# Kernel optimization log

Hardware: AMD Instinct MI355X
Metric: run time of the kernel (lower is better)

Reference implementation:

```python
import jax, jax.numpy as jnp
import numpy as np

I, H, C = 1024, 1024, 1000
B, S = 128, 256


def setup_inputs() -> dict:
    key = jax.random.key(0)
    ks = jax.random.split(key, 7)
    s = 1.0 / np.sqrt(H)
    u = lambda k, shape: jax.random.uniform(k, shape, jnp.float32, -s, s)
    return {
        "x": jax.random.normal(ks[0], (B, S, I), jnp.float32),
        "Wxh": u(ks[1], (4 * H, I)),   # nn.Linear(input, 4H).weight
        "bxh": u(ks[2], (4 * H,)),
        "Whh": u(ks[3], (4 * H, H)),   # nn.Linear(hidden, 4H).weight
        "bhh": u(ks[4], (4 * H,)),
        "Wfc": jax.random.normal(ks[5], (C, H), jnp.float32) / np.sqrt(H),
        "bfc": jnp.zeros((C,), jnp.float32),
    }


def reference(x, Wxh, bxh, Whh, bhh, Wfc, bfc):
    # x: [B, S, I]. Precompute input projection for all timesteps (one big GEMM).
    xW = jnp.einsum("bsi,gi->sbg", x, Wxh) + bxh + bhh  # [S, B, 4H]

    def step(carry, xw_t):
        h, c = carry
        gates = xw_t + h @ Whh.T               # [B, 4H]
        gi, gf, gg, go = jnp.split(gates, 4, axis=1)  # chunk order: i, f, chat, o
        it = jax.nn.sigmoid(gi)
        ft = jax.nn.sigmoid(gf)
        ot = jax.nn.sigmoid(go)
        chat = jnp.tanh(gg)
        c_new = c * ft + it * chat
        h_new = ot * jnp.tanh(c_new)
        return (h_new, c_new), None

    h0 = jnp.zeros((x.shape[0], H), x.dtype)
    c0 = jnp.zeros((x.shape[0], H), x.dtype)
    (h_last, _), _ = jax.lax.scan(step, (h0, c0), xW)
    return h_last @ Wfc.T + bfc  # [B, C]
```

## Files before the change

kernel.cpp:

```cpp
#include <hip/hip_runtime.h>
#include <hip/hip_bf16.h>

typedef __attribute__((ext_vector_type(8))) short short8;
typedef __attribute__((ext_vector_type(4))) float f32x4;
typedef unsigned long long u64;
typedef unsigned int u32;

#define SQLEN 256
#define BATCH 128
#define HID   1024
#define G4    4096
#define NCLS  1000

static __device__ __forceinline__ float sigm(float x){ return 1.0f/(1.0f+__expf(-x)); }
static __device__ __forceinline__ float tanhx(float x){ return 2.0f/(1.0f+__expf(-2.0f*x)) - 1.0f; }
static __device__ __forceinline__ short bf16b(float x){
  __hip_bfloat16 h = __float2bfloat16(x);
  return __builtin_bit_cast(short, h);
}
static __device__ __forceinline__ float bf2f(short s){
  return __bfloat162float(__builtin_bit_cast(__hip_bfloat16, s));
}

__global__ void cast_x_kernel(const float* __restrict__ x, short* __restrict__ xbf){
  int r = blockIdx.x;
  int s = r >> 7, b = r & 127;
  const float* src = x + ((size_t)b*SQLEN + s)*HID;
  short* dst = xbf + (size_t)r*HID;
  int k = threadIdx.x*4;
  float4 v = *(const float4*)(src + k);
  short4 o; o.x=bf16b(v.x); o.y=bf16b(v.y); o.z=bf16b(v.z); o.w=bf16b(v.w);
  *(short4*)(dst + k) = o;
}

__global__ void cast_w_kernel(const float* __restrict__ src, short* __restrict__ dst){
  int i = (blockIdx.x*256 + threadIdx.x)*4;
  float4 v = *(const float4*)(src + i);
  short4 o; o.x=bf16b(v.x); o.y=bf16b(v.y); o.z=bf16b(v.z); o.w=bf16b(v.w);
  *(short4*)(dst + i) = o;
}

__global__ void bias_kernel(const float* __restrict__ a, const float* __restrict__ b,
                            float* __restrict__ o){
  int i = blockIdx.x*256 + threadIdx.x;
  o[i] = a[i] + b[i];
}

__global__ __launch_bounds__(256,3) void gemm_xw_kernel(
    const short* __restrict__ A, const short* __restrict__ B,
    const float* __restrict__ bias, short* __restrict__ C)
{
  __shared__ __align__(16) short As[4096];
  __shared__ __align__(16) short Bs[4096];
  const int tid = threadIdx.x;
  const int swz = (((int)blockIdx.x & 7) << 10) + ((int)blockIdx.x >> 3);
  const int bm = swz >> 5;
  const int bn = swz & 31;
  const size_t r0 = (size_t)bm*128, n0 = (size_t)bn*128;
  const int lane = tid & 63, wave = tid >> 6;
  const int wm = (wave>>1)*64, wn = (wave&1)*64;
  const int l15 = lane & 15, quad = lane >> 4;

  f32x4 acc[4][4];
  #pragma unroll
  for (int m=0;m<4;++m)
    #pragma unroll
    for (int n=0;n<4;++n) acc[m][n] = (f32x4)0.0f;

  const int c0 = wave*64 + lane;
  const int c1 = c0 + 256;

  for (int kk = 0; kk < 32; ++kk){
    const int k0 = kk*32;
    __syncthreads();
    __builtin_amdgcn_global_load_lds(
        (const void*)(A + (r0 + (c0>>2))*HID + k0 + (c0&3)*8),
        (void*)((char*)As + wave*1024), 16, 0, 0);
    __builtin_amdgcn_global_load_lds(
        (const void*)(A + (r0 + (c1>>2))*HID + k0 + (c1&3)*8),
        (void*)((char*)As + 4096 + wave*1024), 16, 0, 0);
    __builtin_amdgcn_global_load_lds(
        (const void*)(B + (n0 + (c0>>2))*HID + k0 + (c0&3)*8),
        (void*)((char*)Bs + wave*1024), 16, 0, 0);
    __builtin_amdgcn_global_load_lds(
        (const void*)(B + (n0 + (c1>>2))*HID + k0 + (c1&3)*8),
        (void*)((char*)Bs + 4096 + wave*1024), 16, 0, 0);
    __syncthreads();
    short8 af[4], bf[4];
    #pragma unroll
    for (int m=0;m<4;++m) af[m] = *(const short8*)(As + (wm + m*16 + l15)*32 + quad*8);
    #pragma unroll
    for (int n=0;n<4;++n) bf[n] = *(const short8*)(Bs + (wn + n*16 + l15)*32 + quad*8);
    #pragma unroll
    for (int m=0;m<4;++m)
      #pragma unroll
      for (int n=0;n<4;++n)
        acc[m][n] = __builtin_amdgcn_mfma_f32_16x16x32_bf16(af[m], bf[n], acc[m][n], 0,0,0);
  }
  #pragma unroll
  for (int n=0;n<4;++n){
    int s = (int)n0 + wn + n*16;
    float bs = bias[s + l15];
    int g = s >> 10, jgi = (s & 1023) >> 4;
    #pragma unroll
    for (int m=0;m<4;++m){
      #pragma unroll
      for (int rg=0; rg<4; ++rg){
        u32 w0 = (u32)(unsigned short)bf16b(acc[m][n][rg] + bs);
        u32 w1 = __shfl_down(w0, 1);
        u32 w2 = __shfl_down(w0, 2);
        u32 w3 = __shfl_down(w0, 3);
        if ((l15 & 3) == 0){
          u64 pk = (u64)w0 | ((u64)w1<<16) | ((u64)w2<<32) | ((u64)w3<<48);
          int rowin = wm + m*16 + quad*4 + rg;
          *(u64*)(C + (((size_t)bm*64 + jgi)*128 + rowin)*64 + g*16 + l15) = pk;
        }
      }
    }
  }
}

__global__ __launch_bounds__(256,2) void lstm_kernel(
    const short* __restrict__ whh, const short* __restrict__ xw,
    short* __restrict__ h_all, u32* __restrict__ flags)
{
  __shared__ f32x4 part[2][4][4][64];

  const int tid  = threadIdx.x;
  const int lane = tid & 63;
  const int wave = tid >> 6;
  const int l15  = lane & 15;
  const int quad = lane >> 4;
  const int bg = blockIdx.x & 7;
  const int jg = blockIdx.x >> 3;
  const int b0 = bg*16;
  const int j0 = jg*16;
  const int ks0 = wave*256;

  __builtin_amdgcn_fence(__ATOMIC_ACQUIRE, "agent");

  short8 Bf[4][8];
  #pragma unroll
  for (int g=0; g<4; ++g)
    #pragma unroll
    for (int kit=0; kit<8; ++kit)
      Bf[g][kit] = *(const short8*)(whh + (size_t)(g*1024 + j0 + l15)*HID
                                    + ks0 + kit*32 + quad*8);

  u32* fgrp = flags + bg*64;

  const int r  = tid >> 4;
  const int jj = tid & 15;
  const int ln = (r>>2)*16 + jj;
  const int rg = r & 3;
  float cc = 0.0f;

  short xwc[4];
  {
    const short* xb = xw + (((size_t)0*64 + jg)*128 + b0 + r)*64 + jj;
    #pragma unroll
    for (int g=0; g<4; ++g) xwc[g] = xb[g*16];
  }

  for (int t = 0; t < SQLEN; ++t){
    const short* hin  = h_all + (size_t)t*131072;
    short*       hout = h_all + (size_t)(t+1)*131072;

    short xwn[4];
    if (t < SQLEN-1){
      const short* xb = xw + (((size_t)(t+1)*64 + jg)*128 + b0 + r)*64 + jj;
      #pragma unroll
      for (int g=0; g<4; ++g) xwn[g] = xb[g*16];
    }

    if (t){
      u32* fp = fgrp + wave*16 + l15;
      while (__hip_atomic_load(fp, __ATOMIC_RELAXED,
                               __HIP_MEMORY_SCOPE_AGENT) < (u32)t)
        __builtin_amdgcn_s_sleep(1);
      asm volatile("" ::: "memory");
    }

    short8 Af[8];
    #pragma unroll
    for (int kit=0; kit<8; ++kit)
      Af[kit] = *(const short8*)(hin + (size_t)(b0 + l15)*HID
                                 + ks0 + kit*32 + quad*8);

    f32x4 acc[4];
    #pragma unroll
    for (int g=0; g<4; ++g) acc[g] = (f32x4)0.0f;
    #pragma unroll
    for (int kit=0; kit<8; ++kit)
      #pragma unroll
      for (int g=0; g<4; ++g)
        acc[g] = __builtin_amdgcn_mfma_f32_16x16x32_bf16(Af[kit], Bf[g][kit], acc[g],0,0,0);

    const int pb = t & 1;
    #pragma unroll
    for (int g=0; g<4; ++g) part[pb][wave][g][lane] = acc[g];
    __syncthreads();

    float gv[4];
    #pragma unroll
    for (int g=0; g<4; ++g){
      float s = bf2f(xwc[g]);
      #pragma unroll
      for (int w=0; w<4; ++w)
        s += ((const float*)&part[pb][w][g][ln])[rg];
      gv[g] = s;
    }

    float it = sigm(gv[0]), ft = sigm(gv[1]), ch = tanhx(gv[2]), ot = sigm(gv[3]);
    cc = cc*ft + it*ch;
    float hv = ot * tanhx(cc);

    u32 w0 = (u32)(unsigned short)bf16b(hv);
    u32 w1 = __shfl_down(w0, 1);
    u32 w2 = __shfl_down(w0, 2);
    u32 w3 = __shfl_down(w0, 3);
    if (!(tid & 3)){
      u64 hp = (u64)w0 | ((u64)w1<<16) | ((u64)w2<<32) | ((u64)w3<<48);
      __hip_atomic_store((u64*)(hout + (size_t)(b0 + r)*HID + j0 + jj), hp,
                         __ATOMIC_RELAXED, __HIP_MEMORY_SCOPE_AGENT);
    }
    xwc[0]=xwn[0]; xwc[1]=xwn[1]; xwc[2]=xwn[2]; xwc[3]=xwn[3];
    __syncthreads();

    if (t < SQLEN-1 && tid == 0)
      __hip_atomic_store(fgrp + jg, (u32)(t+1), __ATOMIC_RELAXED,
                         __HIP_MEMORY_SCOPE_AGENT);
  }
}

__global__ __launch_bounds__(256) void fc_kernel(const short* __restrict__ h,
    const float* __restrict__ wfc, const float* __restrict__ bfc, float* __restrict__ out)
{
  __shared__ float hs[4][1024];
  int tid = threadIdx.x;
  int b0 = (blockIdx.x >> 3)*4;
  int cs = (blockIdx.x & 7)*125;
  for (int i = tid; i < 4096; i += 256){
    int bb = i >> 10, k = i & 1023;
    hs[bb][k] = bf2f(h[(size_t)(b0+bb)*HID + k]);
  }
  __syncthreads();
  for (int c = cs + tid; c < cs + 125; c += 256){
    const float* w = wfc + (size_t)c*HID;
    float a0=0.f,a1=0.f,a2=0.f,a3=0.f;
    for (int k=0; k<1024; k+=4){
      float4 wv = *(const float4*)(w + k);
      a0 += wv.x*hs[0][k] + wv.y*hs[0][k+1] + wv.z*hs[0][k+2] + wv.w*hs[0][k+3];
      a1 += wv.x*hs[1][k] + wv.y*hs[1][k+1] + wv.z*hs[1][k+2] + wv.w*hs[1][k+3];
      a2 += wv.x*hs[2][k] + wv.y*hs[2][k+1] + wv.z*hs[2][k+2] + wv.w*hs[2][k+3];
      a3 += wv.x*hs[3][k] + wv.y*hs[3][k+1] + wv.z*hs[3][k+2] + wv.w*hs[3][k+3];
    }
    float bb = bfc[c];
    out[(size_t)(b0+0)*NCLS + c] = a0 + bb;
    out[(size_t)(b0+1)*NCLS + c] = a1 + bb;
    out[(size_t)(b0+2)*NCLS + c] = a2 + bb;
    out[(size_t)(b0+3)*NCLS + c] = a3 + bb;
  }
}

extern "C" void kernel_launch(void* const* d_in, const int* in_sizes, int n_in,
                              void* d_out, int out_size, void* d_ws, size_t ws_size,
                              hipStream_t stream) {
  const float* x   = (const float*)d_in[0];
  const float* Wxh = (const float*)d_in[1];
  const float* bxh = (const float*)d_in[2];
  const float* Whh = (const float*)d_in[3];
  const float* bhh = (const float*)d_in[4];
  const float* Wfc = (const float*)d_in[5];
  const float* bfc = (const float*)d_in[6];
  float* out = (float*)d_out;

  char* ws = (char*)d_ws;
  short*    h_all = (short*)(ws + 0);
  short*    xbf   = (short*)(ws + 0);
  short*    wxhb  = (short*)(ws + 68157440);
  short*    whhb  = (short*)(ws + 76546048);
  float*    biasg = (float*)(ws + 84934656);
  short*    xw    = (short*)(ws + 85983232);
  u32*      flags = (u32*)(ws + 354418688);

  hipMemsetAsync(flags, 0, 4096, stream);

  cast_x_kernel<<<32768, 256, 0, stream>>>(x, xbf);
  cast_w_kernel<<<4096, 256, 0, stream>>>(Wxh, wxhb);
  cast_w_kernel<<<4096, 256, 0, stream>>>(Whh, whhb);
  bias_kernel  <<<16,   256, 0, stream>>>(bxh, bhh, biasg);
  gemm_xw_kernel<<<8192, 256, 0, stream>>>(xbf, wxhb, biasg, xw);
  hipMemsetAsync(ws, 0, 262144, stream);
  lstm_kernel  <<<512,  256, 0, stream>>>(whhb, xw, h_all, flags);
  fc_kernel    <<<256,  256, 0, stream>>>(h_all + (size_t)SQLEN*131072, Wfc, bfc, out);
}
```

Baseline: 1.599 ms.

## Enlarge xW GEMM tiles to 256x256 with double-buffered LDS prefetch

Rewrites the input-projection GEMM to use 512-thread blocks computing 256x256 output tiles with a K-step of 64. Global-to-LDS loads are double-buffered, so the next two K tiles are staged while the current one is computed, synchronised with explicit waitcnt and barrier instructions. Fragments are stored in MFMA-ready order so LDS reads are contiguous per lane. The aim is more data reuse per load and overlap of memory with MFMA work, at the cost of 128 KB of LDS and more accumulator registers per thread, which limits occupancy.

```diff
diff --git a/kernel.cpp b/kernel.cpp
--- a/kernel.cpp
+++ b/kernel.cpp
@@ -46,64 +46,91 @@
   o[i] = a[i] + b[i];
 }
 
-__global__ __launch_bounds__(256,3) void gemm_xw_kernel(
+__global__ __launch_bounds__(512,2) void gemm_xw_kernel(
     const short* __restrict__ A, const short* __restrict__ B,
     const float* __restrict__ bias, short* __restrict__ C)
 {
-  __shared__ __align__(16) short As[4096];
-  __shared__ __align__(16) short Bs[4096];
-  const int tid = threadIdx.x;
-  const int swz = (((int)blockIdx.x & 7) << 10) + ((int)blockIdx.x >> 3);
-  const int bm = swz >> 5;
-  const int bn = swz & 31;
-  const size_t r0 = (size_t)bm*128, n0 = (size_t)bn*128;
-  const int lane = tid & 63, wave = tid >> 6;
-  const int wm = (wave>>1)*64, wn = (wave&1)*64;
-  const int l15 = lane & 15, quad = lane >> 4;
-
-  f32x4 acc[4][4];
+  __shared__ __align__(16) short As[2][16384];
+  __shared__ __align__(16) short Bs[2][16384];
+  const int tid  = threadIdx.x;
+  const int lane = tid & 63;
+  const int wave = tid >> 6;
+  const int l15  = lane & 15;
+  const int quad = lane >> 4;
+  const int swz = (((int)blockIdx.x & 7) << 8) + ((int)blockIdx.x >> 3);
+  const int bm = swz >> 4;
+  const int bn = swz & 15;
+  const size_t r0 = (size_t)bm*256, n0 = (size_t)bn*256;
+  const int wmr = wave >> 2;
+  const int wnc = wave & 3;
+
+  f32x4 acc[8][4];
   #pragma unroll
-  for (int m=0;m<4;++m)
+  for (int m=0;m<8;++m)
     #pragma unroll
     for (int n=0;n<4;++n) acc[m][n] = (f32x4)0.0f;
 
-  const int c0 = wave*64 + lane;
-  const int c1 = c0 + 256;
-
-  for (int kk = 0; kk < 32; ++kk){
-    const int k0 = kk*32;
-    __syncthreads();
-    __builtin_amdgcn_global_load_lds(
-        (const void*)(A + (r0 + (c0>>2))*HID + k0 + (c0&3)*8),
-        (void*)((char*)As + wave*1024), 16, 0, 0);
-    __builtin_amdgcn_global_load_lds(
-        (const void*)(A + (r0 + (c1>>2))*HID + k0 + (c1&3)*8),
-        (void*)((char*)As + 4096 + wave*1024), 16, 0, 0);
-    __builtin_amdgcn_global_load_lds(
-        (const void*)(B + (n0 + (c0>>2))*HID + k0 + (c0&3)*8),
-        (void*)((char*)Bs + wave*1024), 16, 0, 0);
-    __builtin_amdgcn_global_load_lds(
-        (const void*)(B + (n0 + (c1>>2))*HID + k0 + (c1&3)*8),
-        (void*)((char*)Bs + 4096 + wave*1024), 16, 0, 0);
-    __syncthreads();
-    short8 af[4], bf[4];
-    #pragma unroll
-    for (int m=0;m<4;++m) af[m] = *(const short8*)(As + (wm + m*16 + l15)*32 + quad*8);
-    #pragma unroll
-    for (int n=0;n<4;++n) bf[n] = *(const short8*)(Bs + (wn + n*16 + l15)*32 + quad*8);
-    #pragma unroll
-    for (int m=0;m<4;++m)
+  auto stage = [&](int buf, int kt){
+    const int k0 = kt*64;
+    #pragma unroll
+    for (int r=0;r<4;++r){
+      const int fa = r*8 + wave, m = fa>>1, kit = fa&1;
+      __builtin_amdgcn_global_load_lds(
+        (const void*)(A + (r0 + m*16 + l15)*HID + k0 + kit*32 + quad*8),
+        (void*)((char*)&As[buf][0] + r*8192 + wave*1024), 16, 0, 0);
+    }
+    #pragma unroll
+    for (int r=0;r<4;++r){
+      const int fb = r*8 + wave, n = fb>>1, kit = fb&1;
+      __builtin_amdgcn_global_load_lds(
+        (const void*)(B + (n0 + n*16 + l15)*HID + k0 + kit*32 + quad*8),
+        (void*)((char*)&Bs[buf][0] + r*8192 + wave*1024), 16, 0, 0);
+    }
+  };
+  auto compute = [&](int buf){
+    #pragma unroll
+    for (int kit=0;kit<2;++kit){
+      short8 a[8], b[4];
+      #pragma unroll
+      for (int m=0;m<8;++m)
+        a[m] = *(const short8*)((char*)&As[buf][0]
+                                + ((wmr*8 + m)*2 + kit)*1024 + lane*16);
       #pragma unroll
       for (int n=0;n<4;++n)
-        acc[m][n] = __builtin_amdgcn_mfma_f32_16x16x32_bf16(af[m], bf[n], acc[m][n], 0,0,0);
-  }
+        b[n] = *(const short8*)((char*)&Bs[buf][0]
+                                + ((wnc*4 + n)*2 + kit)*1024 + lane*16);
+      #pragma unroll
+      for (int m=0;m<8;++m)
+        #pragma unroll
+        for (int n=0;n<4;++n)
+          acc[m][n] = __builtin_amdgcn_mfma_f32_16x16x32_bf16(a[m], b[n], acc[m][n], 0,0,0);
+    }
+  };
+
+  stage(0, 0);
+  stage(1, 1);
+  asm volatile("s_waitcnt vmcnt(8)\n\ts_barrier" ::: "memory");
+
+  for (int kt = 0; kt < 16; ++kt){
+    compute(kt & 1);
+    asm volatile("s_waitcnt lgkmcnt(0)\n\ts_barrier" ::: "memory");
+    if (kt + 2 < 16) stage(kt & 1, kt + 2);
+    if (kt + 1 < 16){
+      if (kt + 2 < 16)
+        asm volatile("s_waitcnt vmcnt(8)\n\ts_barrier" ::: "memory");
+      else
+        asm volatile("s_waitcnt vmcnt(0)\n\ts_barrier" ::: "memory");
+    }
+  }
+
+  const int s_idx = bm*2 + wmr;
   #pragma unroll
   for (int n=0;n<4;++n){
-    int s = (int)n0 + wn + n*16;
+    int s = (int)n0 + wnc*64 + n*16;
     float bs = bias[s + l15];
     int g = s >> 10, jgi = (s & 1023) >> 4;
     #pragma unroll
-    for (int m=0;m<4;++m){
+    for (int m=0;m<8;++m){
       #pragma unroll
       for (int rg=0; rg<4; ++rg){
         u32 w0 = (u32)(unsigned short)bf16b(acc[m][n][rg] + bs);
@@ -112,8 +139,8 @@
         u32 w3 = __shfl_down(w0, 3);
         if ((l15 & 3) == 0){
           u64 pk = (u64)w0 | ((u64)w1<<16) | ((u64)w2<<32) | ((u64)w3<<48);
-          int rowin = wm + m*16 + quad*4 + rg;
-          *(u64*)(C + (((size_t)bm*64 + jgi)*128 + rowin)*64 + g*16 + l15) = pk;
+          int b = m*16 + quad*4 + rg;
+          *(u64*)(C + (((size_t)s_idx*64 + jgi)*128 + b)*64 + g*16 + l15) = pk;
         }
       }
     }
@@ -290,7 +317,7 @@
   cast_w_kernel<<<4096, 256, 0, stream>>>(Wxh, wxhb);
   cast_w_kernel<<<4096, 256, 0, stream>>>(Whh, whhb);
   bias_kernel  <<<16,   256, 0, stream>>>(bxh, bhh, biasg);
-  gemm_xw_kernel<<<8192, 256, 0, stream>>>(xbf, wxhb, biasg, xw);
+  gemm_xw_kernel<<<2048, 512, 0, stream>>>(xbf, wxhb, biasg, xw);
   hipMemsetAsync(ws, 0, 262144, stream);
   lstm_kernel  <<<512,  256, 0, stream>>>(whhb, xw, h_all, flags);
   fc_kernel    <<<256,  256, 0, stream>>>(h_all + (size_t)SQLEN*131072, Wfc, bfc, out);
```

After: 1.648 ms. +3.1%, slower.

## Fuse input-projection GEMM with LSTM recurrence into one persistent kernel

Applied to the files above, without the earlier changes.

Merges the xW GEMM and the LSTM recurrence into a single launch. Blocks 0-511 run the recurrence and blocks 512-1023 run the GEMM in timestep order, bumping a per-timestep counter when each tile is stored. LSTM blocks spin on that counter before reading the projection for the next timestep, so the projection overlaps the serial recurrence. This needs all 1024 blocks to be co-resident to avoid deadlock, and GEMM blocks compete with the latency-critical recurrence for compute units and bandwidth. h_all moves to a separate buffer so it no longer aliases xbf.

```diff
diff --git a/kernel.cpp b/kernel.cpp
--- a/kernel.cpp
+++ b/kernel.cpp
@@ -9,7 +9,6 @@
 #define SQLEN 256
 #define BATCH 128
 #define HID   1024
-#define G4    4096
 #define NCLS  1000
 
 static __device__ __forceinline__ float sigm(float x){ return 1.0f/(1.0f+__expf(-x)); }
@@ -46,93 +45,103 @@
   o[i] = a[i] + b[i];
 }
 
-__global__ __launch_bounds__(256,3) void gemm_xw_kernel(
-    const short* __restrict__ A, const short* __restrict__ B,
-    const float* __restrict__ bias, short* __restrict__ C)
+__global__ __launch_bounds__(256,4) void mega_kernel(
+    const short* __restrict__ xbf, const short* __restrict__ wxh,
+    const float* __restrict__ bias, const short* __restrict__ whh,
+    short* __restrict__ xw, short* __restrict__ h_all,
+    u32* __restrict__ flags, u32* __restrict__ gcnt)
 {
-  __shared__ __align__(16) short As[4096];
-  __shared__ __align__(16) short Bs[4096];
+  __shared__ __align__(16) char smem_u[32768];
+  const int bid = (int)blockIdx.x;
   const int tid = threadIdx.x;
-  const int swz = (((int)blockIdx.x & 7) << 10) + ((int)blockIdx.x >> 3);
-  const int bm = swz >> 5;
-  const int bn = swz & 31;
-  const size_t r0 = (size_t)bm*128, n0 = (size_t)bn*128;
   const int lane = tid & 63, wave = tid >> 6;
-  const int wm = (wave>>1)*64, wn = (wave&1)*64;
   const int l15 = lane & 15, quad = lane >> 4;
 
-  f32x4 acc[4][4];
-  #pragma unroll
-  for (int m=0;m<4;++m)
-    #pragma unroll
-    for (int n=0;n<4;++n) acc[m][n] = (f32x4)0.0f;
-
-  const int c0 = wave*64 + lane;
-  const int c1 = c0 + 256;
-
-  for (int kk = 0; kk < 32; ++kk){
-    const int k0 = kk*32;
-    __syncthreads();
-    __builtin_amdgcn_global_load_lds(
-        (const void*)(A + (r0 + (c0>>2))*HID + k0 + (c0&3)*8),
-        (void*)((char*)As + wave*1024), 16, 0, 0);
-    __builtin_amdgcn_global_load_lds(
-        (const void*)(A + (r0 + (c1>>2))*HID + k0 + (c1&3)*8),
-        (void*)((char*)As + 4096 + wave*1024), 16, 0, 0);
-    __builtin_amdgcn_global_load_lds(
-        (const void*)(B + (n0 + (c0>>2))*HID + k0 + (c0&3)*8),
-        (void*)((char*)Bs + wave*1024), 16, 0, 0);
-    __builtin_amdgcn_global_load_lds(
-        (const void*)(B + (n0 + (c1>>2))*HID + k0 + (c1&3)*8),
-        (void*)((char*)Bs + 4096 + wave*1024), 16, 0, 0);
-    __syncthreads();
-    short8 af[4], bf[4];
-    #pragma unroll
-    for (int m=0;m<4;++m) af[m] = *(const short8*)(As + (wm + m*16 + l15)*32 + quad*8);
-    #pragma unroll
-    for (int n=0;n<4;++n) bf[n] = *(const short8*)(Bs + (wn + n*16 + l15)*32 + quad*8);
-    #pragma unroll
-    for (int m=0;m<4;++m)
-      #pragma unroll
-      for (int n=0;n<4;++n)
-        acc[m][n] = __builtin_amdgcn_mfma_f32_16x16x32_bf16(af[m], bf[n], acc[m][n], 0,0,0);
-  }
-  #pragma unroll
-  for (int n=0;n<4;++n){
-    int s = (int)n0 + wn + n*16;
-    float bs = bias[s + l15];
-    int g = s >> 10, jgi = (s & 1023) >> 4;
-    #pragma unroll
-    for (int m=0;m<4;++m){
-      #pragma unroll
-      for (int rg=0; rg<4; ++rg){
-        u32 w0 = (u32)(unsigned short)bf16b(acc[m][n][rg] + bs);
-        u32 w1 = __shfl_down(w0, 1);
-        u32 w2 = __shfl_down(w0, 2);
-        u32 w3 = __shfl_down(w0, 3);
-        if ((l15 & 3) == 0){
-          u64 pk = (u64)w0 | ((u64)w1<<16) | ((u64)w2<<32) | ((u64)w3<<48);
-          int rowin = wm + m*16 + quad*4 + rg;
-          *(u64*)(C + (((size_t)bm*64 + jgi)*128 + rowin)*64 + g*16 + l15) = pk;
+  if (bid >= 512){
+    short* As = (short*)smem_u;
+    short* Bs = (short*)(smem_u + 8192);
+    const int g = bid - 512;
+    const int wm = (wave>>1)*64, wn = (wave&1)*64;
+    const int c0 = wave*64 + lane;
+    const int c1 = c0 + 256;
+    const int local = ((g & 7) << 6) + (g >> 3);
+    const int bn  = local & 31;
+    const int bmi = local >> 5;
+    const size_t n0 = (size_t)bn*128;
+
+    #pragma unroll 1
+    for (int r = 0; r < 16; ++r){
+      const int bm = r*16 + bmi;
+      const size_t r0 = (size_t)bm*128;
+      f32x4 acc[4][4];
+      #pragma unroll
+      for (int m=0;m<4;++m)
+        #pragma unroll
+        for (int n=0;n<4;++n) acc[m][n] = (f32x4)0.0f;
+
+      #pragma unroll 1
+      for (int kk = 0; kk < 32; ++kk){
+        const int k0 = kk*32;
+        __syncthreads();
+        __builtin_amdgcn_global_load_lds(
+            (const void*)(xbf + (r0 + (c0>>2))*HID + k0 + (c0&3)*8),
+            (void*)(As + wave*512), 16, 0, 0);
+        __builtin_amdgcn_global_load_lds(
+            (const void*)(xbf + (r0 + (c1>>2))*HID + k0 + (c1&3)*8),
+            (void*)(As + 2048 + wave*512), 16, 0, 0);
+        __builtin_amdgcn_global_load_lds(
+            (const void*)(wxh + (n0 + (c0>>2))*HID + k0 + (c0&3)*8),
+            (void*)(Bs + wave*512), 16, 0, 0);
+        __builtin_amdgcn_global_load_lds(
+            (const void*)(wxh + (n0 + (c1>>2))*HID + k0 + (c1&3)*8),
+            (void*)(Bs + 2048 + wave*512), 16, 0, 0);
+        __syncthreads();
+        short8 af[4], bf[4];
+        #pragma unroll
+        for (int m=0;m<4;++m) af[m] = *(const short8*)(As + (wm + m*16 + l15)*32 + quad*8);
+        #pragma unroll
+        for (int n=0;n<4;++n) bf[n] = *(const short8*)(Bs + (wn + n*16 + l15)*32 + quad*8);
+        #pragma unroll
+        for (int m=0;m<4;++m)
+          #pragma unroll
+          for (int n=0;n<4;++n)
+            acc[m][n] = __builtin_amdgcn_mfma_f32_16x16x32_bf16(af[m], bf[n], acc[m][n], 0,0,0);
+      }
+      #pragma unroll
+      for (int n=0;n<4;++n){
+        int s = (int)n0 + wn + n*16;
+        float bs = bias[s + l15];
+        int gg = s >> 10, jgi = (s & 1023) >> 4;
+        #pragma unroll
+        for (int m=0;m<4;++m){
+          #pragma unroll
+          for (int rg=0; rg<4; ++rg){
+            u32 w0 = (u32)(unsigned short)bf16b(acc[m][n][rg] + bs);
+            u32 w1 = __shfl_down(w0, 1);
+            u32 w2 = __shfl_down(w0, 2);
+            u32 w3 = __shfl_down(w0, 3);
+            if ((l15 & 3) == 0){
+              u64 pk = (u64)w0 | ((u64)w1<<16) | ((u64)w2<<32) | ((u64)w3<<48);
+              int rowin = wm + m*16 + quad*4 + rg;
+              __hip_atomic_store(
+                (u64*)(xw + (((size_t)bm*64 + jgi)*128 + rowin)*64 + gg*16 + l15),
+                pk, __ATOMIC_RELAXED, __HIP_MEMORY_SCOPE_AGENT);
+            }
+          }
         }
       }
-    }
-  }
-}
-
-__global__ __launch_bounds__(256,2) void lstm_kernel(
-    const short* __restrict__ whh, const short* __restrict__ xw,
-    short* __restrict__ h_all, u32* __restrict__ flags)
-{
-  __shared__ f32x4 part[2][4][4][64];
-
-  const int tid  = threadIdx.x;
-  const int lane = tid & 63;
-  const int wave = tid >> 6;
-  const int l15  = lane & 15;
-  const int quad = lane >> 4;
-  const int bg = blockIdx.x & 7;
-  const int jg = blockIdx.x >> 3;
+      __syncthreads();
+      if (tid == 0)
+        __hip_atomic_fetch_add(gcnt + bm, 1u, __ATOMIC_RELAXED,
+                               __HIP_MEMORY_SCOPE_AGENT);
+    }
+    return;
+  }
+
+  f32x4 (*part)[4][4][64] = reinterpret_cast<f32x4(*)[4][4][64]>(smem_u);
+
+  const int bg = bid & 7;
+  const int jg = bid >> 3;
   const int b0 = bg*16;
   const int j0 = jg*16;
   const int ks0 = wave*256;
@@ -157,6 +166,10 @@
 
   short xwc[4];
   {
+    while (__hip_atomic_load(gcnt + 0, __ATOMIC_RELAXED,
+                             __HIP_MEMORY_SCOPE_AGENT) < 32u)
+      __builtin_amdgcn_s_sleep(1);
+    asm volatile("" ::: "memory");
     const short* xb = xw + (((size_t)0*64 + jg)*128 + b0 + r)*64 + jj;
     #pragma unroll
     for (int g=0; g<4; ++g) xwc[g] = xb[g*16];
@@ -168,6 +181,10 @@
 
     short xwn[4];
     if (t < SQLEN-1){
+      while (__hip_atomic_load(gcnt + (t+1), __ATOMIC_RELAXED,
+                               __HIP_MEMORY_SCOPE_AGENT) < 32u)
+        __builtin_amdgcn_s_sleep(1);
+      asm volatile("" ::: "memory");
       const short* xb = xw + (((size_t)(t+1)*64 + jg)*128 + b0 + r)*64 + jj;
       #pragma unroll
       for (int g=0; g<4; ++g) xwn[g] = xb[g*16];
@@ -276,22 +293,23 @@
   float* out = (float*)d_out;
 
   char* ws = (char*)d_ws;
-  short*    h_all = (short*)(ws + 0);
   short*    xbf   = (short*)(ws + 0);
   short*    wxhb  = (short*)(ws + 68157440);
   short*    whhb  = (short*)(ws + 76546048);
   float*    biasg = (float*)(ws + 84934656);
   short*    xw    = (short*)(ws + 85983232);
-  u32*      flags = (u32*)(ws + 354418688);
-
-  hipMemsetAsync(flags, 0, 4096, stream);
+  short*    h_all = (short*)(ws + 354418688);
+  u32*      flags = (u32*)(ws + 421789696);
+  u32*      gcnt  = (u32*)(ws + 421793792);
+
+  hipMemsetAsync(flags, 0, 8192, stream);
 
   cast_x_kernel<<<32768, 256, 0, stream>>>(x, xbf);
   cast_w_kernel<<<4096, 256, 0, stream>>>(Wxh, wxhb);
   cast_w_kernel<<<4096, 256, 0, stream>>>(Whh, whhb);
   bias_kernel  <<<16,   256, 0, stream>>>(bxh, bhh, biasg);
-  gemm_xw_kernel<<<8192, 256, 0, stream>>>(xbf, wxhb, biasg, xw);
-  hipMemsetAsync(ws, 0, 262144, stream);
-  lstm_kernel  <<<512,  256, 0, stream>>>(whhb, xw, h_all, flags);
+  hipMemsetAsync(h_all, 0, 262144, stream);
+  mega_kernel<<<1024, 256, 0, stream>>>(xbf, wxhb, biasg, whhb,
+                                        xw, h_all, flags, gcnt);
   fc_kernel    <<<256,  256, 0, stream>>>(h_all + (size_t)SQLEN*131072, Wfc, bfc, out);
 }
```

Result: slower. 3.219 ms (+101.4%).
